# Kernel optimization log

Hardware: AMD Instinct MI355X
Metric: run time of the kernel (lower is better)

The kernel has to match this reference:

```python
import jax, jax.numpy as jnp
import numpy as np

B, T, V, E, U, OUT = 1024, 64, 30, 128, 512, 20


def _lstm(x, W, Uh, b, reverse=False, return_seq=True):
    """Keras-style LSTM (gate order i,f,g,o). x: [B,T,D]. Returns [B,T,U] or [B,U]."""
    nu = Uh.shape[0]
    if reverse:
        x = x[:, ::-1]
    xz = jnp.einsum('btd,dg->btg', x, W) + b  # [B,T,4U] input projection, precomputed

    def step(carry, z_t):
        h, c = carry
        z = z_t + h @ Uh
        i, f, g, o = jnp.split(z, 4, axis=-1)
        c = jax.nn.sigmoid(f) * c + jax.nn.sigmoid(i) * jnp.tanh(g)
        h = jax.nn.sigmoid(o) * jnp.tanh(c)
        return (h, c), h

    bsz = x.shape[0]
    init = (jnp.zeros((bsz, nu), x.dtype), jnp.zeros((bsz, nu), x.dtype))
    (h_last, _), hs = jax.lax.scan(step, init, jnp.swapaxes(xz, 0, 1))
    if return_seq:
        hs = jnp.swapaxes(hs, 0, 1)  # [B,T,U]
        if reverse:
            hs = hs[:, ::-1]
        return hs
    return h_last


def setup_inputs() -> dict:
    key = jax.random.key(0)
    ks = jax.random.split(key, 14)
    f32 = jnp.float32

    def n(k, shape, s=0.05):
        return jax.random.normal(k, shape, f32) * s

    G = 4 * U
    return {
        'x': jax.random.randint(ks[0], (B, T), 0, V, dtype=jnp.int32),
        'emb': n(ks[1], (V, E)),
        # layer 1 forward / backward directions
        'W1f': n(ks[2], (E, G)), 'U1f': n(ks[3], (U, G)), 'b1f': jnp.zeros((G,), f32),
        'W1b': n(ks[4], (E, G)), 'U1b': n(ks[5], (U, G)), 'b1b': jnp.zeros((G,), f32),
        # layer 2 forward / backward directions (input dim = 2U from concat)
        'W2f': n(ks[6], (2 * U, G)), 'U2f': n(ks[7], (U, G)), 'b2f': jnp.zeros((G,), f32),
        'W2b': n(ks[8], (2 * U, G)), 'U2b': n(ks[9], (U, G)), 'b2b': jnp.zeros((G,), f32),
        # dense head
        'Wd': n(ks[10], (2 * U, 2 * U)), 'bd': jnp.zeros((2 * U,), f32),
        'Wo': n(ks[11], (2 * U, OUT)), 'bo': jnp.zeros((OUT,), f32),
    }


def reference(x, emb, W1f, U1f, b1f, W1b, U1b, b1b,
              W2f, U2f, b2f, W2b, U2b, b2b, Wd, bd, Wo, bo):
    e = emb[x]  # [B,T,E] embedding lookup
    # Bidirectional LSTM 1, return_sequences=True, concat merge -> [B,T,2U]
    h1 = jnp.concatenate([
        _lstm(e, W1f, U1f, b1f),
        _lstm(e, W1b, U1b, b1b, reverse=True),
    ], axis=-1)
    # Bidirectional LSTM 2, return_sequences=False -> [B,2U]
    h2 = jnp.concatenate([
        _lstm(h1, W2f, U2f, b2f, return_seq=False),
        _lstm(h1, W2b, U2b, b2b, reverse=True, return_seq=False),
    ], axis=-1)
    d = jax.nn.relu(h2 @ Wd + bd)  # Dense(2U, relu)
    return d @ Wo + bo             # Dense(output_len), [B,OUT]
```

## Files before the change

kernel.cpp:

```cpp
#include <hip/hip_runtime.h>
#include <hip/hip_bf16.h>

typedef __hip_bfloat16 bf16;
typedef __attribute__((ext_vector_type(4))) float f32x4;
typedef __attribute__((ext_vector_type(8))) short s16x8;

__device__ __forceinline__ float sigf(float x) {
    return 1.0f / (1.0f + __expf(-x));
}
__device__ __forceinline__ float tanh_f(float x) {
    float ax = fabsf(x);
    float e = __expf(-2.0f * ax);
    float r = (1.0f - e) / (1.0f + e);
    return x < 0.0f ? -r : r;
}

#define GLL16(src, ldst)                                                      \
    __builtin_amdgcn_global_load_lds(                                         \
        (const __attribute__((address_space(1))) void*)(src),                 \
        (__attribute__((address_space(3))) void*)(ldst), 16, 0, 0)

__global__ void k_embw(const float* __restrict__ emb,
                       const float* __restrict__ W1f, const float* __restrict__ b1f,
                       const float* __restrict__ W1b, const float* __restrict__ b1b,
                       float* __restrict__ embW) {
    int c = blockIdx.x * 256 + threadIdx.x;
    int v = blockIdx.y;
    int d = blockIdx.z;
    const float* W = d ? W1b : W1f;
    const float* b = d ? b1b : b1f;
    float acc = b[c];
    const float* er = emb + v * 128;
#pragma unroll 8
    for (int e = 0; e < 128; ++e) acc += er[e] * W[e * 2048 + c];
    int n = ((c & 511) << 2) | (c >> 9);
    embW[(d * 30 + v) * 2048 + n] = acc;
}

__global__ void k_b2r(const float* __restrict__ b2f, const float* __restrict__ b2b,
                      float* __restrict__ dst) {
    int i = blockIdx.x * 256 + threadIdx.x;
    int d = i >> 11, n = i & 2047;
    int c = ((n & 3) << 9) | (n >> 2);
    dst[i] = (d ? b2b : b2f)[c];
}

template<int REORDER, int XOR>
__global__ void k_trans(const float* __restrict__ src, bf16* __restrict__ dst,
                        int ncols, int kpitch, int koff) {
    __shared__ float tile[64][65];
    int k0 = blockIdx.x * 64;
    int c0 = blockIdx.y * 64;
    int tid = threadIdx.x;
#pragma unroll
    for (int i = 0; i < 16; ++i) {
        int seg = tid + i * 256;
        int r = seg >> 6, cc = seg & 63;
        tile[r][cc] = src[(size_t)(k0 + r) * ncols + c0 + cc];
    }
    __syncthreads();
#pragma unroll
    for (int i = 0; i < 16; ++i) {
        int seg = tid + i * 256;
        int nl = seg >> 6, kl = seg & 63;
        int c = c0 + nl;
        int n = REORDER ? (((c & 511) << 2) | (c >> 9)) : c;
        int kabs = koff + k0 + kl;
        int ks = XOR ? (kabs ^ ((n & 7) << 3)) : kabs;
        dst[(size_t)n * kpitch + ks] = __float2bfloat16(tile[kl][nl]);
    }
}

template<int MODE>
__global__ __launch_bounds__(256, 2)
void k_step(const bf16* __restrict__ A1, const bf16* __restrict__ A2,
            const bf16* __restrict__ Bt, const float* __restrict__ table,
            const int* __restrict__ xin, float* __restrict__ c_st,
            bf16* __restrict__ h_out, bf16* __restrict__ h1s, int t)
{
    constexpr int NCH = (MODE == 0) ? 8 : 24;
    constexpr int BP  = (MODE == 0) ? 512 : 1536;

    __shared__ __align__(16) short ldss[24576];

    const int tid  = threadIdx.x;
    const int lane = tid & 63;
    const int wv   = tid >> 6;
    const int wm   = wv << 5;

    const int xcd = blockIdx.x & 7, idx = blockIdx.x >> 3;
    const int n0  = ((xcd << 2) | (idx >> 4)) << 6;
    const int m0  = (idx & 15) << 7;

    const int dir = (m0 >= 1024);
    const int t_a = dir ? 63 - t : t;
    const int rl  = lane & 15;
    const int q8  = (lane >> 4) << 3;
    const int q4  = (lane >> 4) << 2;
    const int xk  = (rl & 7) << 3;
    const int u0  = n0 >> 2;

    const char* a1b;
    if constexpr (MODE == 1)
        a1b = (const char*)(A1 + ((size_t)t_a << 20) + ((size_t)(m0 & 1023) << 10));
    else
        a1b = (const char*)(A1 + (size_t)m0 * 512);
    const char* const btb = (const char*)(Bt + ((size_t)dir * 2048 + n0) * BP);
    const char* const a2b = (const char*)A2;

    auto stage = [&](int c, int buf) {
        char* base = (char*)ldss + buf * 24576;
#pragma unroll
        for (int i = 0; i < 4; ++i) {
            const int u = i * 256 + tid;
            const int r = u >> 3, j = u & 7;
            const char* src;
            if constexpr (MODE == 0)
                src = a1b + r * 1024 + c * 128 + j * 16;
            else
                src = (c < 16) ? a1b + r * 2048 + c * 128 + j * 16
                               : a2b + (size_t)(m0 + r) * 1024 + (c - 16) * 128 + j * 16;
            GLL16(src, base + (i * 256 + wv * 64) * 16);
        }
#pragma unroll
        for (int i = 0; i < 2; ++i) {
            const int u = i * 256 + tid;
            const int r = u >> 3, j = u & 7;
            GLL16(btb + (size_t)r * (BP * 2) + c * 128 + j * 16,
                  base + 16384 + (i * 256 + wv * 64) * 16);
        }
    };

    f32x4 acc[2][4];
#pragma unroll
    for (int i = 0; i < 2; ++i)
#pragma unroll
        for (int j = 0; j < 4; ++j) acc[i][j] = (f32x4){0.f, 0.f, 0.f, 0.f};

    stage(0, 0);

    for (int c = 0; c < NCH; ++c) {
        __syncthreads();
        if (c + 1 < NCH) stage(c + 1, (c + 1) & 1);
        const short* as = ldss + (c & 1) * 12288;
        const short* bs = as + 8192;
#pragma unroll
        for (int ks = 0; ks < 2; ++ks) {
            const int eo = ((ks << 5) + q8) ^ xk;
            s16x8 af[2], bq[4];
#pragma unroll
            for (int f = 0; f < 2; ++f)
                af[f] = *(const s16x8*)&as[(wm + f * 16 + rl) * 64 + eo];
#pragma unroll
            for (int f = 0; f < 4; ++f)
                bq[f] = *(const s16x8*)&bs[(f * 16 + rl) * 64 + eo];
#pragma unroll
            for (int fm = 0; fm < 2; ++fm)
#pragma unroll
                for (int fn = 0; fn < 4; ++fn)
                    acc[fm][fn] = __builtin_amdgcn_mfma_f32_16x16x32_bf16(
                        af[fm], bq[fn], acc[fm][fn], 0, 0, 0);
        }
    }

    float* z = (float*)ldss;
    __syncthreads();
#pragma unroll
    for (int fm = 0; fm < 2; ++fm)
#pragma unroll
        for (int fn = 0; fn < 4; ++fn) {
            const int zr = wm + fm * 16 + q4;
            const int zc = fn * 16 + rl;
#pragma unroll
            for (int r = 0; r < 4; ++r)
                z[(zr + r) * 68 + zc] = acc[fm][fn][r];
        }
    __syncthreads();
#pragma unroll 2
    for (int j = 0; j < 8; ++j) {
        const int cid = j * 256 + tid;
        const int ml = cid >> 4;
        const int ul = cid & 15;
        const int mg = m0 + ml;
        const int b  = mg & 1023;
        float4 z4 = *(float4*)&z[ml * 68 + (ul << 2)];
        const float* tab;
        if constexpr (MODE == 0) {
            const int v = xin[(b << 6) + t_a];
            tab = table + (size_t)(dir * 30 + v) * 2048;
        } else {
            tab = table + dir * 2048;
        }
        const float4 tv = *(const float4*)&tab[n0 + (ul << 2)];
        const float zi = z4.x + tv.x, zf = z4.y + tv.y;
        const float zg = z4.z + tv.z, zo = z4.w + tv.w;
        const float ig = sigf(zi), fg = sigf(zf);
        const float gg = tanh_f(zg), og = sigf(zo);
        const int u = u0 + ul;
        const size_t cu = (size_t)mg * 512 + u;
        const float cn = fg * c_st[cu] + ig * gg;
        c_st[cu] = cn;
        const float h = og * tanh_f(cn);
        const int us = u ^ ((mg & 7) << 3);
        h_out[(size_t)mg * 512 + us] = __float2bfloat16(h);
        if constexpr (MODE == 0) {
            const int col = (((dir << 9) | u) ^ ((b & 7) << 3));
            h1s[(((size_t)t_a << 10) + b) * 1024 + col] = __float2bfloat16(h);
        }
    }
}

__global__ __launch_bounds__(256, 2)
void k_dense(const bf16* __restrict__ hin, const bf16* __restrict__ Bt,
             const float* __restrict__ bd, bf16* __restrict__ dbuf)
{
    __shared__ __align__(16) short ldss[32768];
    const int tid  = threadIdx.x;
    const int lane = tid & 63;
    const int wv   = tid >> 6;
    const int wm   = (wv >> 1) << 6;
    const int wn   = (wv & 1) << 6;
    const int n0   = (blockIdx.x & 7) << 7;
    const int m0   = (blockIdx.x >> 3) << 7;

    const char* const a1b = (const char*)(hin + (size_t)m0 * 512);
    const char* const a2b = (const char*)(hin + (size_t)1024 * 512);
    const char* const btb = (const char*)(Bt + (size_t)n0 * 1024);

    auto stage = [&](int c, int buf) {
#pragma unroll
        for (int i = 0; i < 4; ++i) {
            const int u = i * 256 + tid;
            const int r = u >> 3, j = u & 7;
            const char* src = (c < 8)
                ? a1b + r * 1024 + c * 128 + j * 16
                : a2b + (size_t)(m0 + r) * 1024 + (c - 8) * 128 + j * 16;
            GLL16(src, (char*)ldss + buf * 16384 + (i * 256 + wv * 64) * 16);
        }
#pragma unroll
        for (int i = 0; i < 4; ++i) {
            const int u = i * 256 + tid;
            const int r = u >> 3, j = u & 7;
            GLL16(btb + (size_t)r * 2048 + c * 128 + j * 16,
                  (char*)ldss + 32768 + buf * 16384 + (i * 256 + wv * 64) * 16);
        }
    };

    f32x4 acc[4][4];
#pragma unroll
    for (int i = 0; i < 4; ++i)
#pragma unroll
        for (int j = 0; j < 4; ++j) acc[i][j] = (f32x4){0.f, 0.f, 0.f, 0.f};

    stage(0, 0);
    const int rl = lane & 15;
    const int q8 = (lane >> 4) << 3;
    const int xk = (rl & 7) << 3;

#pragma unroll 2
    for (int c = 0; c < 16; ++c) {
        __syncthreads();
        if (c + 1 < 16) stage(c + 1, (c + 1) & 1);
        const short* as = ldss + (c & 1) * 8192;
        const short* bs = ldss + 16384 + (c & 1) * 8192;
#pragma unroll
        for (int ks = 0; ks < 2; ++ks) {
            const int eo = ((ks << 5) + q8) ^ xk;
            s16x8 af[4], bq[4];
#pragma unroll
            for (int f = 0; f < 4; ++f)
                af[f] = *(const s16x8*)&as[(wm + f * 16 + rl) * 64 + eo];
#pragma unroll
            for (int f = 0; f < 4; ++f)
                bq[f] = *(const s16x8*)&bs[(wn + f * 16 + rl) * 64 + eo];
#pragma unroll
            for (int fm = 0; fm < 4; ++fm)
#pragma unroll
                for (int fn = 0; fn < 4; ++fn)
                    acc[fm][fn] = __builtin_amdgcn_mfma_f32_16x16x32_bf16(
                        af[fm], bq[fn], acc[fm][fn], 0, 0, 0);
        }
    }

#pragma unroll
    for (int fn = 0; fn < 4; ++fn) {
        const int col = n0 + wn + fn * 16 + rl;
        const float bdv = bd[col];
#pragma unroll
        for (int fm = 0; fm < 4; ++fm) {
            const int rb = m0 + wm + fm * 16 + ((lane >> 4) << 2);
#pragma unroll
            for (int r = 0; r < 4; ++r) {
                float v = acc[fm][fn][r] + bdv;
                dbuf[(size_t)(rb + r) * 1024 + col] =
                    __float2bfloat16(v > 0.f ? v : 0.f);
            }
        }
    }
}

__global__ __launch_bounds__(256)
void k_out(const bf16* __restrict__ dbuf, const float* __restrict__ Wo,
           const float* __restrict__ bo, float* __restrict__ out) {
    int b = blockIdx.x, tid = threadIdx.x;
    int wv = tid >> 6, lane = tid & 63;
    float acc[5] = {0.f, 0.f, 0.f, 0.f, 0.f};
    for (int kk = 0; kk < 1024; kk += 64) {
        float a = __bfloat162float(dbuf[b * 1024 + kk + lane]);
#pragma unroll
        for (int j = 0; j < 5; ++j)
            acc[j] += a * Wo[(kk + lane) * 20 + wv + j * 4];
    }
#pragma unroll
    for (int j = 0; j < 5; ++j) {
        float s = acc[j];
        for (int off = 32; off; off >>= 1) s += __shfl_down(s, off, 64);
        if (lane == 0) out[b * 20 + wv + j * 4] = s + bo[wv + j * 4];
    }
}

extern "C" void kernel_launch(void* const* d_in, const int* in_sizes, int n_in,
                              void* d_out, int out_size, void* d_ws, size_t ws_size,
                              hipStream_t stream) {
    const int*   x   = (const int*)  d_in[0];
    const float* emb = (const float*)d_in[1];
    const float* W1f = (const float*)d_in[2];
    const float* U1f = (const float*)d_in[3];
    const float* b1f = (const float*)d_in[4];
    const float* W1b = (const float*)d_in[5];
    const float* U1b = (const float*)d_in[6];
    const float* b1b = (const float*)d_in[7];
    const float* W2f = (const float*)d_in[8];
    const float* U2f = (const float*)d_in[9];
    const float* b2f = (const float*)d_in[10];
    const float* W2b = (const float*)d_in[11];
    const float* U2b = (const float*)d_in[12];
    const float* b2b = (const float*)d_in[13];
    const float* Wd  = (const float*)d_in[14];
    const float* bd  = (const float*)d_in[15];
    const float* Wo  = (const float*)d_in[16];
    const float* bo  = (const float*)d_in[17];

    char* ws = (char*)d_ws;
    float* embW = (float*)(ws + 0);
    float* b2r  = (float*)(ws + 491520);
    bf16* Ut1   = (bf16*)(ws + 507904);
    bf16* BigBt = (bf16*)(ws + 4702208);
    bf16* Wdt   = (bf16*)(ws + 17285120);
    bf16* hA    = (bf16*)(ws + 19382272);
    bf16* hB    = (bf16*)(ws + 21479424);
    float* cst  = (float*)(ws + 23576576);
    bf16* dbuf  = (bf16*)(ws + 27770880);
    bf16* h1seq = (bf16*)(ws + 29868032);

    k_embw<<<dim3(8, 30, 2), 256, 0, stream>>>(emb, W1f, b1f, W1b, b1b, embW);
    k_b2r<<<16, 256, 0, stream>>>(b2f, b2b, b2r);
    k_trans<1, 1><<<dim3(8, 32), 256, 0, stream>>>(U1f, Ut1,              2048, 512, 0);
    k_trans<1, 1><<<dim3(8, 32), 256, 0, stream>>>(U1b, Ut1 + 2048 * 512, 2048, 512, 0);
    k_trans<1, 1><<<dim3(16, 32), 256, 0, stream>>>(W2f, BigBt,                2048, 1536, 0);
    k_trans<1, 1><<<dim3(8, 32), 256, 0, stream>>>(U2f, BigBt,                2048, 1536, 1024);
    k_trans<1, 1><<<dim3(16, 32), 256, 0, stream>>>(W2b, BigBt + 2048 * 1536, 2048, 1536, 0);
    k_trans<1, 1><<<dim3(8, 32), 256, 0, stream>>>(U2b, BigBt + 2048 * 1536, 2048, 1536, 1024);
    k_trans<0, 1><<<dim3(16, 16), 256, 0, stream>>>(Wd, Wdt, 1024, 1024, 0);

    hipMemsetAsync(hA, 0, (size_t)2048 * 512 * sizeof(bf16), stream);
    hipMemsetAsync(cst, 0, (size_t)2048 * 512 * sizeof(float), stream);
    bf16 *hin = hA, *hout = hB;
    for (int t = 0; t < 64; ++t) {
        k_step<0><<<512, 256, 0, stream>>>(
            hin, (const bf16*)nullptr, Ut1, embW, x, cst, hout, h1seq, t);
        bf16* tmp = hin; hin = hout; hout = tmp;
    }

    hipMemsetAsync(hin, 0, (size_t)2048 * 512 * sizeof(bf16), stream);
    hipMemsetAsync(cst, 0, (size_t)2048 * 512 * sizeof(float), stream);
    for (int t = 0; t < 64; ++t) {
        k_step<1><<<512, 256, 0, stream>>>(
            h1seq, hin, BigBt, b2r, (const int*)nullptr, cst, hout,
            (bf16*)nullptr, t);
        bf16* tmp = hin; hin = hout; hout = tmp;
    }

    k_dense<<<64, 256, 0, stream>>>(hin, Wdt, bd, dbuf);
    k_out<<<1024, 256, 0, stream>>>(dbuf, Wo, bo, (float*)d_out);
}
```

Before: 2.170 ms.

## Triple-buffer LDS staging in LSTM step GEMM with partial vmcnt waits

Moves the step GEMM from a double-buffered LDS pipeline to a triple-buffered one. Two chunks are prefetched ahead, and each barrier waits only for the older chunk's global_load_lds through a partial s_waitcnt vmcnt, with s_setprio raised around the MFMA block. The goal is to hide global-to-LDS latency behind compute. LDS per block grows to 72 KB through dynamic shared memory, which may reduce blocks per CU, and the hand-written vmcnt count must match the number of loads issued per stage.

Measured after the change: 2.204 ms. About the same (+1.6%).

```diff
diff --git a/kernel.cpp b/kernel.cpp
--- a/kernel.cpp
+++ b/kernel.cpp
@@ -19,6 +19,13 @@
     __builtin_amdgcn_global_load_lds(                                         \
         (const __attribute__((address_space(1))) void*)(src),                 \
         (__attribute__((address_space(3))) void*)(ldst), 16, 0, 0)
+
+#define PIPE_BAR(N)                                                           \
+    do {                                                                      \
+        asm volatile("s_waitcnt vmcnt(" #N ") lgkmcnt(0)" ::: "memory");      \
+        __builtin_amdgcn_s_barrier();                                         \
+        __builtin_amdgcn_sched_barrier(0);                                    \
+    } while (0)
 
 __global__ void k_embw(const float* __restrict__ emb,
                        const float* __restrict__ W1f, const float* __restrict__ b1f,
@@ -81,7 +88,7 @@
     constexpr int NCH = (MODE == 0) ? 8 : 24;
     constexpr int BP  = (MODE == 0) ? 512 : 1536;
 
-    __shared__ __align__(16) short ldss[24576];
+    extern __shared__ __align__(16) short ldss[];
 
     const int tid  = threadIdx.x;
     const int lane = tid & 63;
@@ -137,13 +144,9 @@
 #pragma unroll
         for (int j = 0; j < 4; ++j) acc[i][j] = (f32x4){0.f, 0.f, 0.f, 0.f};
 
-    stage(0, 0);
-
-    for (int c = 0; c < NCH; ++c) {
-        __syncthreads();
-        if (c + 1 < NCH) stage(c + 1, (c + 1) & 1);
-        const short* as = ldss + (c & 1) * 12288;
+    auto compute = [&](const short* as) {
         const short* bs = as + 8192;
+        __builtin_amdgcn_s_setprio(1);
 #pragma unroll
         for (int ks = 0; ks < 2; ++ks) {
             const int eo = ((ks << 5) + q8) ^ xk;
@@ -161,7 +164,23 @@
                     acc[fm][fn] = __builtin_amdgcn_mfma_f32_16x16x32_bf16(
                         af[fm], bq[fn], acc[fm][fn], 0, 0, 0);
         }
-    }
+        __builtin_amdgcn_s_setprio(0);
+    };
+
+    stage(0, 0);
+    stage(1, 1);
+
+    int cb = 0, sb = 2;
+#pragma unroll 1
+    for (int c = 0; c < NCH - 1; ++c) {
+        PIPE_BAR(6);
+        if (c + 2 < NCH) stage(c + 2, sb);
+        compute(ldss + cb * 12288);
+        cb = (cb == 2) ? 0 : cb + 1;
+        sb = (sb == 2) ? 0 : sb + 1;
+    }
+    PIPE_BAR(0);
+    compute(ldss + cb * 12288);
 
     float* z = (float*)ldss;
     __syncthreads();
@@ -353,6 +372,11 @@
     bf16* dbuf  = (bf16*)(ws + 27770880);
     bf16* h1seq = (bf16*)(ws + 29868032);
 
+    hipFuncSetAttribute((const void*)k_step<0>,
+                        hipFuncAttributeMaxDynamicSharedMemorySize, 73728);
+    hipFuncSetAttribute((const void*)k_step<1>,
+                        hipFuncAttributeMaxDynamicSharedMemorySize, 73728);
+
     k_embw<<<dim3(8, 30, 2), 256, 0, stream>>>(emb, W1f, b1f, W1b, b1b, embW);
     k_b2r<<<16, 256, 0, stream>>>(b2f, b2b, b2r);
     k_trans<1, 1><<<dim3(8, 32), 256, 0, stream>>>(U1f, Ut1,              2048, 512, 0);
@@ -367,7 +391,7 @@
     hipMemsetAsync(cst, 0, (size_t)2048 * 512 * sizeof(float), stream);
     bf16 *hin = hA, *hout = hB;
     for (int t = 0; t < 64; ++t) {
-        k_step<0><<<512, 256, 0, stream>>>(
+        k_step<0><<<512, 256, 73728, stream>>>(
             hin, (const bf16*)nullptr, Ut1, embW, x, cst, hout, h1seq, t);
         bf16* tmp = hin; hin = hout; hout = tmp;
     }
@@ -375,7 +399,7 @@
     hipMemsetAsync(hin, 0, (size_t)2048 * 512 * sizeof(bf16), stream);
     hipMemsetAsync(cst, 0, (size_t)2048 * 512 * sizeof(float), stream);
     for (int t = 0; t < 64; ++t) {
-        k_step<1><<<512, 256, 0, stream>>>(
+        k_step<1><<<512, 256, 73728, stream>>>(
             h1seq, hin, BigBt, b2r, (const int*)nullptr, cst, hout,
             (bf16*)nullptr, t);
         bf16* tmp = hin; hin = hout; hout = tmp;
```
